# Kernel tuning notes

Measured on AMD Instinct MI355X. Metric: run time of the kernel, lower is better.

The kernel has to match this reference:

```python
import jax, jax.numpy as jnp
import numpy as np

INPUT_DIM = 32
HIDDEN = 512
ACTION_DIM = 4
NUM_OBJ = 10
BATCH = 1024
LN_EPS = 1e-5


def _edge_list(B, K):
    # fully connected, no self loops, row-major like torch.nonzero
    adj = np.ones((K, K), dtype=np.int64) - np.eye(K, dtype=np.int64)
    e = np.argwhere(adj)                      # [K*(K-1), 2]
    e = np.tile(e, (B, 1))
    off = np.repeat(np.arange(B, dtype=np.int64) * K, K * (K - 1))
    e = e + off[:, None]
    return jnp.asarray(e[:, 0]), jnp.asarray(e[:, 1])  # row, col


def _layer_norm(x, g, b):
    m = x.mean(-1, keepdims=True)
    v = x.var(-1, keepdims=True)
    return (x - m) / jnp.sqrt(v + LN_EPS) * g + b


def _mlp(x, w1, b1, w2, b2, g, bt, w3, b3):
    h = jax.nn.relu(x @ w1 + b1)
    h = jax.nn.relu(_layer_norm(h @ w2 + b2, g, bt))
    return h @ w3 + b3


def setup_inputs() -> dict:
    key = jax.random.key(0)
    ks = jax.random.split(key, 16)

    def lin(k, i, o):
        return jax.random.normal(k, (i, o), jnp.float32) / np.sqrt(i)

    states = jax.random.normal(ks[0], (BATCH, NUM_OBJ, INPUT_DIM), jnp.float32)
    action = jax.random.randint(ks[1], (BATCH,), 0, ACTION_DIM, jnp.int64)

    node_in = HIDDEN + INPUT_DIM + ACTION_DIM  # 548
    return {
        "states": states, "action": action,
        # edge MLP: 2*input_dim -> hidden
        "ew1": lin(ks[2], 2 * INPUT_DIM, HIDDEN), "eb1": jnp.zeros((HIDDEN,), jnp.float32),
        "ew2": lin(ks[3], HIDDEN, HIDDEN),        "eb2": jnp.zeros((HIDDEN,), jnp.float32),
        "eg": jnp.ones((HIDDEN,), jnp.float32),   "ebt": jnp.zeros((HIDDEN,), jnp.float32),
        "ew3": lin(ks[4], HIDDEN, HIDDEN),        "eb3": jnp.zeros((HIDDEN,), jnp.float32),
        # node MLP: (input + action + hidden) -> input_dim
        "nw1": lin(ks[5], node_in, HIDDEN),       "nb1": jnp.zeros((HIDDEN,), jnp.float32),
        "nw2": lin(ks[6], HIDDEN, HIDDEN),        "nb2": jnp.zeros((HIDDEN,), jnp.float32),
        "ng": jnp.ones((HIDDEN,), jnp.float32),   "nbt": jnp.zeros((HIDDEN,), jnp.float32),
        "nw3": lin(ks[7], HIDDEN, INPUT_DIM),     "nb3": jnp.zeros((INPUT_DIM,), jnp.float32),
    }


def reference(states, action, ew1, eb1, ew2, eb2, eg, ebt, ew3, eb3,
              nw1, nb1, nw2, nb2, ng, nbt, nw3, nb3):
    B, K, D = states.shape
    node_attr = states.reshape(-1, D)                      # [B*K, D]

    row, col = _edge_list(B, K)
    edge_in = jnp.concatenate([node_attr[row], node_attr[col]], axis=1)  # [E, 2D]
    edge_attr = _mlp(edge_in, ew1, eb1, ew2, eb2, eg, ebt, ew3, eb3)     # [E, H]
    agg = jax.ops.segment_sum(edge_attr, row, num_segments=B * K)       # [B*K, H]

    # copy_action=True, 1-D action: one-hot, same vector for each object
    oh = jax.nn.one_hot(action, ACTION_DIM, dtype=jnp.float32)          # [B, A]
    action_vec = jnp.tile(oh, (1, K)).reshape(-1, ACTION_DIM)           # [B*K, A]

    node_in = jnp.concatenate([node_attr, action_vec, agg], axis=1)     # [B*K, D+A+H]
    out = _mlp(node_in, nw1, nb1, nw2, nb2, ng, nbt, nw3, nb3)          # [B*K, D]
    return out.reshape(B, K, D)
```

## Files before the change

### kernel.cpp

```cpp
#include <hip/hip_runtime.h>

#define HID 512
#define DIN 32
#define KOBJ 10
#define NGRAPH 1024
#define NNODES (NGRAPH*KOBJ)
#define NEDGE (NGRAPH*90)
#define NBLK (NEDGE/64)
#define LN_EPS 1e-5f

typedef __bf16 bf16x8 __attribute__((ext_vector_type(8)));
typedef unsigned short u16x8 __attribute__((ext_vector_type(8)));
typedef unsigned short u16x4 __attribute__((ext_vector_type(4)));
typedef float f32x4 __attribute__((ext_vector_type(4)));

__device__ __forceinline__ unsigned short f2bf(float f) {
    unsigned u = __builtin_bit_cast(unsigned, f);
    u += 0x7fffu + ((u >> 16) & 1u);
    return (unsigned short)(u >> 16);
}
__device__ __forceinline__ float bf2f(unsigned short h) {
    unsigned u = ((unsigned)h) << 16;
    return __builtin_bit_cast(float, u);
}
__device__ __forceinline__ void gl_lds16(const void* g, void* l) {
    __builtin_amdgcn_global_load_lds(
        (__attribute__((address_space(1))) void*)g,
        (__attribute__((address_space(3))) void*)l, 16, 0, 0);
}

__global__ void megapack(const float* __restrict__ ew1, const float* __restrict__ ew2,
                         const float* __restrict__ nw1, const float* __restrict__ nw2,
                         const float* __restrict__ nw3,
                         unsigned short* __restrict__ ew1p, unsigned short* __restrict__ ew2p,
                         unsigned short* __restrict__ nw1p, unsigned short* __restrict__ nw2p,
                         unsigned short* __restrict__ nw3p)
{
    int idx = blockIdx.x * 256 + threadIdx.x;
    if (idx < 32768) {
        int j = idx & 7, c = (idx >> 3) & 1023, kb = idx >> 13;
        int k = kb * 8 + j;
        float v = (c < 512) ? ew1[(size_t)k * 512 + c]
                            : ew1[(size_t)(32 + k) * 512 + (c - 512)];
        ew1p[idx] = f2bf(v);
    } else if (idx < 32768 + 262144) {
        int i = idx - 32768;
        int j = i & 7, c = (i >> 3) & 511, kb = i >> 12;
        ew2p[i] = f2bf(ew2[(size_t)(kb * 8 + j) * 512 + c]);
    } else if (idx < 294912 + 294912) {
        int i = idx - 294912;
        int j = i & 7, c = (i >> 3) & 511, kb = i >> 12;
        int k = kb * 8 + j;
        int sk = (k < 36) ? k : (k < 64 ? -1 : k - 28);
        nw1p[i] = f2bf(sk < 0 ? 0.f : nw1[(size_t)sk * 512 + c]);
    } else if (idx < 589824 + 262144) {
        int i = idx - 589824;
        int j = i & 7, c = (i >> 3) & 511, kb = i >> 12;
        nw2p[i] = f2bf(nw2[(size_t)(kb * 8 + j) * 512 + c]);
    } else if (idx < 851968 + 16384) {
        int i = idx - 851968;
        int j = i & 7, c2 = (i >> 3) & 31, kb = i >> 8;
        nw3p[i] = f2bf(nw3[(size_t)(kb * 8 + j) * 32 + c2]);
    }
}

__global__ __launch_bounds__(512) void fold_w2(
    const float* __restrict__ ew3, const unsigned short* __restrict__ nw1p,
    const float* __restrict__ nw1, const float* __restrict__ nb1,
    const float* __restrict__ eb3, unsigned short* __restrict__ Wfp,
    float* __restrict__ nbf)
{
    if (blockIdx.x == 32) {
        int c = threadIdx.x;
        if (c < 512) {
            float s = 0.f;
            for (int m = 0; m < 512; ++m)
                s = fmaf(eb3[m], nw1[(size_t)(36 + m) * 512 + c], s);
            nbf[c] = nb1[c] + 9.f * s;
        }
        return;
    }
    const int t = threadIdx.x, w = t >> 6, lane = t & 63;
    const int lr = lane & 15, lg = lane >> 4;
    const int rb = blockIdx.x * 16;
    f32x4 acc[4] = {};
    for (int kc = 0; kc < 16; ++kc) {
        const float* s = ew3 + (size_t)(rb + lr) * 512 + kc * 32 + lg * 8;
        float4 x0 = *(const float4*)s, x1 = *(const float4*)(s + 4);
        u16x8 u;
        u[0] = f2bf(x0.x); u[1] = f2bf(x0.y); u[2] = f2bf(x0.z); u[3] = f2bf(x0.w);
        u[4] = f2bf(x1.x); u[5] = f2bf(x1.y); u[6] = f2bf(x1.z); u[7] = f2bf(x1.w);
        bf16x8 a = __builtin_bit_cast(bf16x8, u);
        const size_t kb = (size_t)(8 + kc * 4 + lg) * 512;
#pragma unroll
        for (int nt = 0; nt < 4; ++nt) {
            int c = w * 64 + nt * 16 + lr;
            bf16x8 b = __builtin_bit_cast(bf16x8, *(const u16x8*)(nw1p + (kb + c) * 8));
            acc[nt] = __builtin_amdgcn_mfma_f32_16x16x32_bf16(a, b, acc[nt], 0, 0, 0);
        }
    }
#pragma unroll
    for (int reg = 0; reg < 4; ++reg)
#pragma unroll
        for (int nt = 0; nt < 4; ++nt) {
            int k = rb + lg * 4 + reg;
            int c = w * 64 + nt * 16 + lr;
            Wfp[((size_t)(k >> 3) * 512 + c) * 8 + (k & 7)] = f2bf(acc[nt][reg]);
        }
}

__global__ __launch_bounds__(256) void pq_xa(
    const float* __restrict__ X, const int* __restrict__ act,
    const unsigned short* __restrict__ ew1p, const unsigned short* __restrict__ nw1p,
    const float* __restrict__ eb1, const float* __restrict__ nbf,
    unsigned short* __restrict__ PQ, unsigned short* __restrict__ Rb)
{
    const int t = threadIdx.x, w = t >> 6, lane = t & 63;
    const int lr = lane & 15, lg = lane >> 4;
    const int rb = blockIdx.x * 32;
    const int mode = blockIdx.y;

    bf16x8 a[2];
#pragma unroll
    for (int m = 0; m < 2; ++m) {
        const float* s = X + (size_t)(rb + m * 16 + lr) * 32 + lg * 8;
        float4 x0 = *(const float4*)s, x1 = *(const float4*)(s + 4);
        u16x8 u;
        u[0] = f2bf(x0.x); u[1] = f2bf(x0.y); u[2] = f2bf(x0.z); u[3] = f2bf(x0.w);
        u[4] = f2bf(x1.x); u[5] = f2bf(x1.y); u[6] = f2bf(x1.z); u[7] = f2bf(x1.w);
        a[m] = __builtin_bit_cast(bf16x8, u);
    }

    if (mode < 2) {
        const int half = mode;
        f32x4 acc[2][8] = {};
#pragma unroll
        for (int nt = 0; nt < 8; ++nt) {
            int col = half * 512 + w * 128 + nt * 16 + lr;
            bf16x8 b = __builtin_bit_cast(bf16x8, *(const u16x8*)(ew1p + ((size_t)lg * 1024 + col) * 8));
            acc[0][nt] = __builtin_amdgcn_mfma_f32_16x16x32_bf16(a[0], b, acc[0][nt], 0, 0, 0);
            acc[1][nt] = __builtin_amdgcn_mfma_f32_16x16x32_bf16(a[1], b, acc[1][nt], 0, 0, 0);
        }
#pragma unroll
        for (int nt = 0; nt < 8; ++nt) {
            int col = w * 128 + nt * 16 + lr;
            float eb = (half == 0) ? eb1[col] : 0.f;
#pragma unroll
            for (int m = 0; m < 2; ++m)
#pragma unroll
                for (int reg = 0; reg < 4; ++reg)
                    PQ[(size_t)(rb + m * 16 + lg * 4 + reg) * 1024 + half * 512 + col]
                        = f2bf(acc[m][nt][reg] + eb);
        }
    } else {
        bf16x8 a1[2];
#pragma unroll
        for (int m = 0; m < 2; ++m) {
            int row = rb + m * 16 + lr;
            u16x8 v = (u16x8)(unsigned short)0;
            if (lg == 0) {
                int ac = act[row / KOBJ];
                v[ac & 3] = (unsigned short)0x3f80;
            }
            a1[m] = __builtin_bit_cast(bf16x8, v);
        }
        f32x4 acc[2][8] = {};
#pragma unroll
        for (int nt = 0; nt < 8; ++nt) {
            int col = w * 128 + nt * 16 + lr;
            bf16x8 b0 = __builtin_bit_cast(bf16x8, *(const u16x8*)(nw1p + ((size_t)lg * 512 + col) * 8));
            bf16x8 b1 = __builtin_bit_cast(bf16x8, *(const u16x8*)(nw1p + ((size_t)(4 + lg) * 512 + col) * 8));
#pragma unroll
            for (int m = 0; m < 2; ++m) {
                acc[m][nt] = __builtin_amdgcn_mfma_f32_16x16x32_bf16(a[m], b0, acc[m][nt], 0, 0, 0);
                acc[m][nt] = __builtin_amdgcn_mfma_f32_16x16x32_bf16(a1[m], b1, acc[m][nt], 0, 0, 0);
            }
        }
#pragma unroll
        for (int nt = 0; nt < 8; ++nt) {
            int col = w * 128 + nt * 16 + lr;
            float bb = nbf[col];
#pragma unroll
            for (int m = 0; m < 2; ++m)
#pragma unroll
                for (int reg = 0; reg < 4; ++reg)
                    Rb[(size_t)(rb + m * 16 + lg * 4 + reg) * 512 + col]
                        = f2bf(acc[m][nt][reg] + bb);
        }
    }
}

__global__ __launch_bounds__(512, 4) void edge_v15(
    const unsigned short* __restrict__ PQ, const unsigned short* __restrict__ ew2p,
    const float* __restrict__ eb2, const float* __restrict__ eg,
    const float* __restrict__ ebt, unsigned short* __restrict__ Spart)
{
    __shared__ __align__(16) char ldsraw[77824];
    __shared__ float sums[64], ssums[64];
    unsigned short* Hcol = (unsigned short*)ldsraw;

    const int t = threadIdx.x, w = t >> 6, lane = t & 63;
    const int lr = lane & 15, lg = lane >> 4;
    const int wr = w >> 2, wc = w & 3;
    const int rb = blockIdx.x * 64;

    if (t < 64) { sums[t] = 0.f; ssums[t] = 0.f; }

    const bool ab = (t < 256);
    const int arow = t >> 2, akg = t & 3;
    const int e = rb + arow;
    const int g = e / 90, le = e - g * 90;
    const int i = le / 9, jj = le - i * 9;
    const int j = jj + (jj >= i);
    const unsigned short* pqP = PQ + ((size_t)(g * KOBJ + i)) * 1024 + akg * 8;
    const unsigned short* pqQ = PQ + ((size_t)(g * KOBJ + j)) * 1024 + 512 + akg * 8;

    u16x8 rp = (u16x8)(unsigned short)0, rq = (u16x8)(unsigned short)0;
    auto loadPQ = [&](int kc) {
        if (ab) {
            rp = *(const u16x8*)(pqP + kc * 32);
            rq = *(const u16x8*)(pqQ + kc * 32);
        }
    };
    auto buildA = [&](int buf) {
        if (ab) {
            u16x8 o;
#pragma unroll
            for (int q = 0; q < 8; ++q)
                o[q] = f2bf(fmaxf(bf2f(rp[q]) + bf2f(rq[q]), 0.f));
            *(u16x8*)(ldsraw + 65536 + buf * 5120 + arow * 80 + akg * 16) = o;
        }
    };
    auto fillB = [&](int kc, int buf) {
        char* Bb = ldsraw + buf * 32768;
#pragma unroll
        for (int RR = 0; RR < 4; ++RR)
            gl_lds16(ew2p + (size_t)kc * 16384 + RR * 4096 + t * 8, Bb + RR * 8192 + w * 1024);
    };

    f32x4 acc[2][8] = {};
    loadPQ(0); buildA(0); loadPQ(1); fillB(0, 0);
    __syncthreads();
    int cur = 0;
    for (int kc = 0; kc < 16; ++kc) {
        if (kc < 15) {
            fillB(kc + 1, cur ^ 1);
            buildA(cur ^ 1);
            if (kc < 14) loadPQ(kc + 2);
        }
        const unsigned short* Ab = (const unsigned short*)(ldsraw + 65536 + cur * 5120);
        const unsigned short* Bb = (const unsigned short*)(ldsraw + cur * 32768);
        bf16x8 a0 = *(const bf16x8*)(Ab + (wr * 32 + lr) * 40 + lg * 8);
        bf16x8 a1 = *(const bf16x8*)(Ab + (wr * 32 + 16 + lr) * 40 + lg * 8);
#pragma unroll
        for (int nt = 0; nt < 8; ++nt) {
            bf16x8 b = *(const bf16x8*)(Bb + ((size_t)lg * 512 + wc * 128 + nt * 16 + lr) * 8);
            acc[0][nt] = __builtin_amdgcn_mfma_f32_16x16x32_bf16(a0, b, acc[0][nt], 0, 0, 0);
            acc[1][nt] = __builtin_amdgcn_mfma_f32_16x16x32_bf16(a1, b, acc[1][nt], 0, 0, 0);
        }
        __syncthreads();
        cur ^= 1;
    }

    float b2[8], gv[8], bb[8];
#pragma unroll
    for (int nt = 0; nt < 8; ++nt) {
        int c = wc * 128 + nt * 16 + lr;
        b2[nt] = eb2[c]; gv[nt] = eg[c]; bb[nt] = ebt[c];
    }
#pragma unroll
    for (int m = 0; m < 2; ++m)
#pragma unroll
        for (int reg = 0; reg < 4; ++reg) {
            float s = 0.f, ss = 0.f;
#pragma unroll
            for (int nt = 0; nt < 8; ++nt) {
                float v = acc[m][nt][reg] + b2[nt];
                acc[m][nt][reg] = v;
                s += v; ss += v * v;
            }
#pragma unroll
            for (int msk = 1; msk < 16; msk <<= 1) {
                s  += __shfl_xor(s,  msk, 64);
                ss += __shfl_xor(ss, msk, 64);
            }
            if (lr == 0) {
                int rl = wr * 32 + m * 16 + lg * 4 + reg;
                atomicAdd(&sums[rl], s);
                atomicAdd(&ssums[rl], ss);
            }
        }
    __syncthreads();

#pragma unroll
    for (int m = 0; m < 2; ++m)
#pragma unroll
        for (int nt = 0; nt < 8; ++nt) {
            int c = wc * 128 + nt * 16 + lr;
            u16x4 o;
#pragma unroll
            for (int reg = 0; reg < 4; ++reg) {
                int rl = wr * 32 + m * 16 + lg * 4 + reg;
                float mean = sums[rl] * (1.f / 512.f);
                float var  = ssums[rl] * (1.f / 512.f) - mean * mean;
                float inv  = rsqrtf(var + LN_EPS);
                float h = fmaxf((acc[m][nt][reg] - mean) * inv * gv[nt] + bb[nt], 0.f);
                o[reg] = f2bf(h);
            }
            *(u16x4*)(&Hcol[c * 72 + wr * 32 + m * 16 + lg * 4]) = o;
        }
    __syncthreads();

    {
        const int n0 = rb / 9;
        f32x4 sacc[4] = {};
#pragma unroll
        for (int kc2 = 0; kc2 < 2; ++kc2) {
            u16x8 ia;
#pragma unroll
            for (int q = 0; q < 8; ++q) {
                int k = kc2 * 32 + lg * 8 + q;
                int node = (rb + k) / 9 - n0;
                ia[q] = (node == lr) ? (unsigned short)0x3F80 : (unsigned short)0;
            }
            bf16x8 af = __builtin_bit_cast(bf16x8, ia);
#pragma unroll
            for (int nt = 0; nt < 4; ++nt) {
                int c = w * 64 + nt * 16 + lr;
                bf16x8 bf = *(const bf16x8*)(&Hcol[c * 72 + kc2 * 32 + lg * 8]);
                sacc[nt] = __builtin_amdgcn_mfma_f32_16x16x32_bf16(af, bf, sacc[nt], 0, 0, 0);
            }
        }
        if (lg < 2) {
            unsigned short* dst = Spart + (size_t)blockIdx.x * 4096;
#pragma unroll
            for (int nt = 0; nt < 4; ++nt)
#pragma unroll
                for (int reg = 0; reg < 4; ++reg) {
                    int node = lg * 4 + reg;
                    int c = w * 64 + nt * 16 + lr;
                    dst[node * 512 + c] = f2bf(sacc[nt][reg]);
                }
        }
    }
}

__global__ __launch_bounds__(256) void gather_s(
    const unsigned short* __restrict__ Spart, unsigned short* __restrict__ S)
{
    int idx = blockIdx.x * 256 + threadIdx.x;
    int n = idx >> 6, c8 = idx & 63;
    int e0 = 9 * n;
    int b1 = e0 >> 6, b2 = (e0 + 8) >> 6;
    int nl1 = n - (b1 * 64) / 9;
    const unsigned short* p1 = Spart + ((size_t)b1 * 8 + nl1) * 512 + c8 * 8;
    u16x8 v1 = *(const u16x8*)p1;
    float x[8];
#pragma unroll
    for (int q = 0; q < 8; ++q) x[q] = bf2f(v1[q]);
    if (b2 != b1) {
        int nl2 = n - (b2 * 64) / 9;
        const unsigned short* p2 = Spart + ((size_t)b2 * 8 + nl2) * 512 + c8 * 8;
        u16x8 v2 = *(const u16x8*)p2;
#pragma unroll
        for (int q = 0; q < 8; ++q) x[q] += bf2f(v2[q]);
    }
    u16x8 o;
#pragma unroll
    for (int q = 0; q < 8; ++q) o[q] = f2bf(x[q]);
    *(u16x8*)(S + (size_t)n * 512 + c8 * 8) = o;
}

__global__ __launch_bounds__(512, 4) void node_hh(
    const unsigned short* __restrict__ S, const unsigned short* __restrict__ Wfp,
    const unsigned short* __restrict__ Rb, unsigned short* __restrict__ Hh)
{
    __shared__ __align__(16) unsigned short Bt[32768];
    __shared__ __align__(16) unsigned short At[2048];
    const int t = threadIdx.x, w = t >> 6, lane = t & 63;
    const int lr = lane & 15, lg = lane >> 4;
    const int rb = blockIdx.x * 32;

    f32x4 acc[2][4] = {};
    for (int kc = 0; kc < 8; ++kc) {
        __syncthreads();
#pragma unroll
        for (int RR = 0; RR < 8; ++RR)
            gl_lds16(Wfp + ((size_t)kc * 4096 + RR * 512 + t) * 8,
                     (char*)Bt + RR * 8192 + w * 1024);
        if (w < 4) {
            int row = t >> 3, cp = t & 7;
            int scol = cp ^ (row & 7);
            gl_lds16(S + (size_t)(rb + row) * 512 + kc * 64 + scol * 8,
                     (char*)At + (t & ~63) * 16);
        }
        __syncthreads();
#pragma unroll
        for (int ks = 0; ks < 2; ++ks) {
            int kidx = ks * 4 + lg;
            bf16x8 a0 = *(const bf16x8*)(At + ( 0 + lr) * 64 + (kidx ^ (lr & 7)) * 8);
            bf16x8 a1 = *(const bf16x8*)(At + (16 + lr) * 64 + (kidx ^ (lr & 7)) * 8);
#pragma unroll
            for (int nt = 0; nt < 4; ++nt) {
                bf16x8 b = *(const bf16x8*)(Bt + ((size_t)kidx * 512 + w * 64 + nt * 16 + lr) * 8);
                acc[0][nt] = __builtin_amdgcn_mfma_f32_16x16x32_bf16(a0, b, acc[0][nt], 0, 0, 0);
                acc[1][nt] = __builtin_amdgcn_mfma_f32_16x16x32_bf16(a1, b, acc[1][nt], 0, 0, 0);
            }
        }
    }
#pragma unroll
    for (int m = 0; m < 2; ++m)
#pragma unroll
        for (int reg = 0; reg < 4; ++reg) {
            int row = rb + m * 16 + lg * 4 + reg;
#pragma unroll
            for (int nt = 0; nt < 4; ++nt) {
                int c = w * 64 + nt * 16 + lr;
                float v = acc[m][nt][reg] + bf2f(Rb[(size_t)row * 512 + c]);
                Hh[(size_t)row * 512 + c] = f2bf(fmaxf(v, 0.f));
            }
        }
}

__global__ __launch_bounds__(512, 4) void node_lo(
    const unsigned short* __restrict__ A, const unsigned short* __restrict__ Wp,
    const float* __restrict__ bias, const float* __restrict__ gamma,
    const float* __restrict__ beta, const unsigned short* __restrict__ nw3p,
    const float* __restrict__ nb3, float* __restrict__ out)
{
    __shared__ __align__(16) char raw[69632];
    __shared__ float sums[32], ssums[32];
    unsigned short* Bt = (unsigned short*)raw;
    unsigned short* At = (unsigned short*)(raw + 65536);
    const int t = threadIdx.x, w = t >> 6, lane = t & 63;
    const int lr = lane & 15, lg = lane >> 4;
    const int rb = blockIdx.x * 32;
    if (t < 32) { sums[t] = 0.f; ssums[t] = 0.f; }

    f32x4 acc[2][4] = {};
    for (int kc = 0; kc < 8; ++kc) {
        __syncthreads();
#pragma unroll
        for (int RR = 0; RR < 8; ++RR)
            gl_lds16(Wp + ((size_t)kc * 4096 + RR * 512 + t) * 8,
                     raw + RR * 8192 + w * 1024);
        if (w < 4) {
            int row = t >> 3, cp = t & 7;
            int scol = cp ^ (row & 7);
            gl_lds16(A + (size_t)(rb + row) * 512 + kc * 64 + scol * 8,
                     raw + 65536 + (t & ~63) * 16);
        }
        __syncthreads();
#pragma unroll
        for (int ks = 0; ks < 2; ++ks) {
            int kidx = ks * 4 + lg;
            bf16x8 a0 = *(const bf16x8*)(At + ( 0 + lr) * 64 + (kidx ^ (lr & 7)) * 8);
            bf16x8 a1 = *(const bf16x8*)(At + (16 + lr) * 64 + (kidx ^ (lr & 7)) * 8);
#pragma unroll
            for (int nt = 0; nt < 4; ++nt) {
                bf16x8 b = *(const bf16x8*)(Bt + ((size_t)kidx * 512 + w * 64 + nt * 16 + lr) * 8);
                acc[0][nt] = __builtin_amdgcn_mfma_f32_16x16x32_bf16(a0, b, acc[0][nt], 0, 0, 0);
                acc[1][nt] = __builtin_amdgcn_mfma_f32_16x16x32_bf16(a1, b, acc[1][nt], 0, 0, 0);
            }
        }
    }

    float bv[4], gv[4], be[4];
#pragma unroll
    for (int nt = 0; nt < 4; ++nt) {
        int c = w * 64 + nt * 16 + lr;
        bv[nt] = bias[c]; gv[nt] = gamma[c]; be[nt] = beta[c];
    }
#pragma unroll
    for (int m = 0; m < 2; ++m)
#pragma unroll
        for (int reg = 0; reg < 4; ++reg) {
            float s = 0.f, ss = 0.f;
#pragma unroll
            for (int nt = 0; nt < 4; ++nt) {
                float v = acc[m][nt][reg] + bv[nt];
                acc[m][nt][reg] = v;
                s += v; ss += v * v;
            }
#pragma unroll
            for (int msk = 1; msk < 16; msk <<= 1) {
                s  += __shfl_xor(s,  msk, 64);
                ss += __shfl_xor(ss, msk, 64);
            }
            if (lr == 0) {
                atomicAdd(&sums [m * 16 + lg * 4 + reg], s);
                atomicAdd(&ssums[m * 16 + lg * 4 + reg], ss);
            }
        }
    __syncthreads();

    unsigned short* Hst = (unsigned short*)raw;
#pragma unroll
    for (int m = 0; m < 2; ++m)
#pragma unroll
        for (int reg = 0; reg < 4; ++reg) {
            int rl = m * 16 + lg * 4 + reg;
            float mean = sums[rl] * (1.f / 512.f);
            float var  = ssums[rl] * (1.f / 512.f) - mean * mean;
            float inv  = rsqrtf(var + LN_EPS);
#pragma unroll
            for (int nt = 0; nt < 4; ++nt) {
                int c = w * 64 + nt * 16 + lr;
                float v = fmaxf((acc[m][reg * 0 + nt][reg] * 0.f + acc[m][nt][reg] - mean) * inv * gv[nt] + be[nt], 0.f);
                Hst[rl * 520 + c] = f2bf(v);
            }
        }
    __syncthreads();

    float* Pp = (float*)(raw + 34816);
    {
        f32x4 acc2[2][2] = {};
#pragma unroll
        for (int kc3 = 0; kc3 < 2; ++kc3) {
            int kbase = w * 64 + kc3 * 32;
            bf16x8 a0 = *(const bf16x8*)(Hst + ( 0 + lr) * 520 + kbase + lg * 8);
            bf16x8 a1 = *(const bf16x8*)(Hst + (16 + lr) * 520 + kbase + lg * 8);
#pragma unroll
            for (int ntt = 0; ntt < 2; ++ntt) {
                int kb = (kbase >> 3) + lg;
                bf16x8 b = __builtin_bit_cast(bf16x8,
                    *(const u16x8*)(nw3p + ((size_t)kb * 32 + ntt * 16 + lr) * 8));
                acc2[0][ntt] = __builtin_amdgcn_mfma_f32_16x16x32_bf16(a0, b, acc2[0][ntt], 0, 0, 0);
                acc2[1][ntt] = __builtin_amdgcn_mfma_f32_16x16x32_bf16(a1, b, acc2[1][ntt], 0, 0, 0);
            }
        }
        __syncthreads();
#pragma unroll
        for (int mt = 0; mt < 2; ++mt)
#pragma unroll
            for (int ntt = 0; ntt < 2; ++ntt)
#pragma unroll
                for (int reg = 0; reg < 4; ++reg) {
                    int row = mt * 16 + lg * 4 + reg;
                    int col = ntt * 16 + lr;
                    Pp[(size_t)w * 1024 + row * 32 + col] = acc2[mt][ntt][reg];
                }
    }
    __syncthreads();

    for (int e2 = t; e2 < 1024; e2 += 512) {
        int row = e2 >> 5, col = e2 & 31;
        float s = 0.f;
#pragma unroll
        for (int ww = 0; ww < 8; ++ww) s += Pp[(size_t)ww * 1024 + e2];
        out[(size_t)(rb + row) * 32 + col] = s + nb3[col];
    }
}

extern "C" void kernel_launch(void* const* d_in, const int* in_sizes, int n_in,
                              void* d_out, int out_size, void* d_ws, size_t ws_size,
                              hipStream_t stream)
{
    const float* states = (const float*)d_in[0];
    const int*   action = (const int*)d_in[1];
    const float* ew1 = (const float*)d_in[2];
    const float* eb1 = (const float*)d_in[3];
    const float* ew2 = (const float*)d_in[4];
    const float* eb2 = (const float*)d_in[5];
    const float* eg  = (const float*)d_in[6];
    const float* ebt = (const float*)d_in[7];
    const float* ew3 = (const float*)d_in[8];
    const float* eb3 = (const float*)d_in[9];
    const float* nw1 = (const float*)d_in[10];
    const float* nb1 = (const float*)d_in[11];
    const float* nw2 = (const float*)d_in[12];
    const float* nb2 = (const float*)d_in[13];
    const float* ng  = (const float*)d_in[14];
    const float* nbt = (const float*)d_in[15];
    const float* nw3 = (const float*)d_in[16];
    const float* nb3 = (const float*)d_in[17];

    char* wsb = (char*)d_ws;
    unsigned short* PQ    = (unsigned short*)(wsb);
    unsigned short* Spart = (unsigned short*)(wsb + 20971520);
    unsigned short* S     = (unsigned short*)(wsb + 32768000);
    unsigned short* Rb    = (unsigned short*)(wsb + 43253760);
    unsigned short* Hh    = (unsigned short*)(wsb + 53739520);
    unsigned short* ew1p  = (unsigned short*)(wsb + 74711040);
    unsigned short* ew2p  = (unsigned short*)(wsb + 74776576);
    unsigned short* nw1p  = (unsigned short*)(wsb + 75300864);
    unsigned short* nw2p  = (unsigned short*)(wsb + 75890688);
    unsigned short* Wfp   = (unsigned short*)(wsb + 76414976);
    float*          nbf   = (float*)         (wsb + 76939264);
    unsigned short* nw3p  = (unsigned short*)(wsb + 76941312);
    float* out = (float*)d_out;

    hipLaunchKernelGGL(megapack, dim3(3392), dim3(256), 0, stream,
                       ew1, ew2, nw1, nw2, nw3, ew1p, ew2p, nw1p, nw2p, nw3p);
    hipLaunchKernelGGL(fold_w2, dim3(33), dim3(512), 0, stream,
                       ew3, nw1p, nw1, nb1, eb3, Wfp, nbf);
    hipLaunchKernelGGL(pq_xa, dim3(320, 3), dim3(256), 0, stream,
                       states, action, ew1p, nw1p, eb1, nbf, PQ, Rb);
    hipLaunchKernelGGL(edge_v15, dim3(NBLK), dim3(512), 0, stream,
                       PQ, ew2p, eb2, eg, ebt, Spart);
    hipLaunchKernelGGL(gather_s, dim3(NNODES * 64 / 256), dim3(256), 0, stream, Spart, S);
    hipLaunchKernelGGL(node_hh, dim3(320), dim3(512), 0, stream, S, Wfp, Rb, Hh);
    hipLaunchKernelGGL(node_lo, dim3(320), dim3(512), 0, stream,
                       Hh, nw2p, nb2, ng, nbt, nw3p, nb3, out);
}
```

Before: 165.0 us.

## Fuse segment gather into node_hh with double-buffered LDS and 64x256 tiles

Removes the separate gather_s kernel by having node_hh load the two Spart partial sums per node directly, add them in registers, and write the bf16 result into LDS as the A tile. It also retiles the GEMM to 64 rows by 256 columns per block on a 160x2 grid and double-buffers A and B in LDS, so the next K chunk loads while the current one computes. This drops a kernel launch and a round trip of S through global memory. The cost is a smaller K step per iteration with more barriers, and the Spart reads are repeated for each column half. It also drops a redundant multiply-by-zero term in node_lo.

```diff
diff --git a/kernel.cpp b/kernel.cpp
--- a/kernel.cpp
+++ b/kernel.cpp
@@ -1,4 +1,5 @@
 #include <hip/hip_runtime.h>
+
 
 #define HID 512
 #define DIN 32
@@ -345,77 +346,90 @@
     }
 }
 
-__global__ __launch_bounds__(256) void gather_s(
-    const unsigned short* __restrict__ Spart, unsigned short* __restrict__ S)
-{
-    int idx = blockIdx.x * 256 + threadIdx.x;
-    int n = idx >> 6, c8 = idx & 63;
-    int e0 = 9 * n;
-    int b1 = e0 >> 6, b2 = (e0 + 8) >> 6;
-    int nl1 = n - (b1 * 64) / 9;
-    const unsigned short* p1 = Spart + ((size_t)b1 * 8 + nl1) * 512 + c8 * 8;
-    u16x8 v1 = *(const u16x8*)p1;
-    float x[8];
-#pragma unroll
-    for (int q = 0; q < 8; ++q) x[q] = bf2f(v1[q]);
-    if (b2 != b1) {
-        int nl2 = n - (b2 * 64) / 9;
-        const unsigned short* p2 = Spart + ((size_t)b2 * 8 + nl2) * 512 + c8 * 8;
-        u16x8 v2 = *(const u16x8*)p2;
-#pragma unroll
-        for (int q = 0; q < 8; ++q) x[q] += bf2f(v2[q]);
-    }
-    u16x8 o;
-#pragma unroll
-    for (int q = 0; q < 8; ++q) o[q] = f2bf(x[q]);
-    *(u16x8*)(S + (size_t)n * 512 + c8 * 8) = o;
-}
-
-__global__ __launch_bounds__(512, 4) void node_hh(
-    const unsigned short* __restrict__ S, const unsigned short* __restrict__ Wfp,
+__global__ __launch_bounds__(512, 4) void node_hh13(
+    const unsigned short* __restrict__ Spart, const unsigned short* __restrict__ Wfp,
     const unsigned short* __restrict__ Rb, unsigned short* __restrict__ Hh)
 {
-    __shared__ __align__(16) unsigned short Bt[32768];
-    __shared__ __align__(16) unsigned short At[2048];
+    __shared__ __align__(16) unsigned short Bsh[2][8192];
+    __shared__ __align__(16) unsigned short Ash[2][2560];
     const int t = threadIdx.x, w = t >> 6, lane = t & 63;
     const int lr = lane & 15, lg = lane >> 4;
-    const int rb = blockIdx.x * 32;
+    const int wr = w >> 2, wc = w & 3;
+    const int rb = blockIdx.x * 64;
+    const int nh = blockIdx.y;
+
+    const bool ab = (t < 256);
+    const int arow = t >> 2, akg = t & 3;
+    const int n = rb + arow;
+    const int e0 = 9 * n;
+    const int b1 = e0 >> 6, b2 = (e0 + 8) >> 6;
+    const int nl1 = n - (b1 * 64) / 9;
+    const int nl2 = n - (b2 * 64) / 9;
+    const unsigned short* p1 = Spart + ((size_t)b1 * 8 + nl1) * 512 + akg * 8;
+    const unsigned short* p2 = Spart + ((size_t)b2 * 8 + nl2) * 512 + akg * 8;
+    const bool two = (b2 != b1);
+
+    u16x8 r1 = (u16x8)(unsigned short)0, r2 = (u16x8)(unsigned short)0;
+    auto loadA = [&](int kc) {
+        if (ab) {
+            r1 = *(const u16x8*)(p1 + kc * 32);
+            if (two) r2 = *(const u16x8*)(p2 + kc * 32);
+        }
+    };
+    auto buildA = [&](int buf) {
+        if (ab) {
+            u16x8 o;
+#pragma unroll
+            for (int q = 0; q < 8; ++q) {
+                float s = bf2f(r1[q]) + (two ? bf2f(r2[q]) : 0.f);
+                o[q] = f2bf(s);
+            }
+            *(u16x8*)(&Ash[buf][arow * 40 + akg * 8]) = o;
+        }
+    };
+    auto fillB = [&](int kc, int buf) {
+        char* Bb = (char*)&Bsh[buf][0];
+#pragma unroll
+        for (int RR = 0; RR < 2; ++RR) {
+            int gi = RR * 512 + t;
+            int kbl = gi >> 8, col = gi & 255;
+            gl_lds16(Wfp + ((size_t)(kc * 4 + kbl) * 512 + nh * 256 + col) * 8,
+                     Bb + RR * 8192 + w * 1024);
+        }
+    };
 
     f32x4 acc[2][4] = {};
-    for (int kc = 0; kc < 8; ++kc) {
+    loadA(0); buildA(0); loadA(1); fillB(0, 0);
+    __syncthreads();
+    int cur = 0;
+    for (int kc = 0; kc < 16; ++kc) {
+        if (kc < 15) {
+            fillB(kc + 1, cur ^ 1);
+            buildA(cur ^ 1);
+            if (kc < 14) loadA(kc + 2);
+        }
+        const unsigned short* Ab = &Ash[cur][0];
+        const unsigned short* Bb = &Bsh[cur][0];
+        bf16x8 a0 = *(const bf16x8*)(Ab + (wr * 32 + lr) * 40 + lg * 8);
+        bf16x8 a1 = *(const bf16x8*)(Ab + (wr * 32 + 16 + lr) * 40 + lg * 8);
+#pragma unroll
+        for (int nt = 0; nt < 4; ++nt) {
+            bf16x8 b = *(const bf16x8*)(Bb + ((size_t)lg * 256 + wc * 64 + nt * 16 + lr) * 8);
+            acc[0][nt] = __builtin_amdgcn_mfma_f32_16x16x32_bf16(a0, b, acc[0][nt], 0, 0, 0);
+            acc[1][nt] = __builtin_amdgcn_mfma_f32_16x16x32_bf16(a1, b, acc[1][nt], 0, 0, 0);
+        }
         __syncthreads();
-#pragma unroll
-        for (int RR = 0; RR < 8; ++RR)
-            gl_lds16(Wfp + ((size_t)kc * 4096 + RR * 512 + t) * 8,
-                     (char*)Bt + RR * 8192 + w * 1024);
-        if (w < 4) {
-            int row = t >> 3, cp = t & 7;
-            int scol = cp ^ (row & 7);
-            gl_lds16(S + (size_t)(rb + row) * 512 + kc * 64 + scol * 8,
-                     (char*)At + (t & ~63) * 16);
-        }
-        __syncthreads();
-#pragma unroll
-        for (int ks = 0; ks < 2; ++ks) {
-            int kidx = ks * 4 + lg;
-            bf16x8 a0 = *(const bf16x8*)(At + ( 0 + lr) * 64 + (kidx ^ (lr & 7)) * 8);
-            bf16x8 a1 = *(const bf16x8*)(At + (16 + lr) * 64 + (kidx ^ (lr & 7)) * 8);
+        cur ^= 1;
+    }
+
+#pragma unroll
+    for (int m = 0; m < 2; ++m)
+#pragma unroll
+        for (int reg = 0; reg < 4; ++reg) {
+            int row = rb + wr * 32 + m * 16 + lg * 4 + reg;
 #pragma unroll
             for (int nt = 0; nt < 4; ++nt) {
-                bf16x8 b = *(const bf16x8*)(Bt + ((size_t)kidx * 512 + w * 64 + nt * 16 + lr) * 8);
-                acc[0][nt] = __builtin_amdgcn_mfma_f32_16x16x32_bf16(a0, b, acc[0][nt], 0, 0, 0);
-                acc[1][nt] = __builtin_amdgcn_mfma_f32_16x16x32_bf16(a1, b, acc[1][nt], 0, 0, 0);
-            }
-        }
-    }
-#pragma unroll
-    for (int m = 0; m < 2; ++m)
-#pragma unroll
-        for (int reg = 0; reg < 4; ++reg) {
-            int row = rb + m * 16 + lg * 4 + reg;
-#pragma unroll
-            for (int nt = 0; nt < 4; ++nt) {
-                int c = w * 64 + nt * 16 + lr;
+                int c = nh * 256 + wc * 64 + nt * 16 + lr;
                 float v = acc[m][nt][reg] + bf2f(Rb[(size_t)row * 512 + c]);
                 Hh[(size_t)row * 512 + c] = f2bf(fmaxf(v, 0.f));
             }
@@ -506,7 +520,7 @@
 #pragma unroll
             for (int nt = 0; nt < 4; ++nt) {
                 int c = w * 64 + nt * 16 + lr;
-                float v = fmaxf((acc[m][reg * 0 + nt][reg] * 0.f + acc[m][nt][reg] - mean) * inv * gv[nt] + be[nt], 0.f);
+                float v = fmaxf((acc[m][nt][reg] - mean) * inv * gv[nt] + be[nt], 0.f);
                 Hst[rl * 520 + c] = f2bf(v);
             }
         }
@@ -578,7 +592,6 @@
     char* wsb = (char*)d_ws;
     unsigned short* PQ    = (unsigned short*)(wsb);
     unsigned short* Spart = (unsigned short*)(wsb + 20971520);
-    unsigned short* S     = (unsigned short*)(wsb + 32768000);
     unsigned short* Rb    = (unsigned short*)(wsb + 43253760);
     unsigned short* Hh    = (unsigned short*)(wsb + 53739520);
     unsigned short* ew1p  = (unsigned short*)(wsb + 74711040);
@@ -598,8 +611,8 @@
                        states, action, ew1p, nw1p, eb1, nbf, PQ, Rb);
     hipLaunchKernelGGL(edge_v15, dim3(NBLK), dim3(512), 0, stream,
                        PQ, ew2p, eb2, eg, ebt, Spart);
-    hipLaunchKernelGGL(gather_s, dim3(NNODES * 64 / 256), dim3(256), 0, stream, Spart, S);
-    hipLaunchKernelGGL(node_hh, dim3(320), dim3(512), 0, stream, S, Wfp, Rb, Hh);
+    hipLaunchKernelGGL(node_hh13, dim3(160, 2), dim3(512), 0, stream,
+                       Spart, Wfp, Rb, Hh);
     hipLaunchKernelGGL(node_lo, dim3(320), dim3(512), 0, stream,
                        Hh, nw2p, nb2, ng, nbt, nw3p, nb3, out);
 }
```

Measured after the change: 162.6 us, median of 2. About the same (-1.4%).
